# Optimization experiments

Measured on AMD Instinct MI355X. Metric: run time of the kernel, lower is better.

Reference implementation:

```python
import jax, jax.numpy as jnp
from jax import lax
import numpy as np

D_MODEL = 1024
D_STATE = 16
D_CONV = 4
EXPAND = 2
D_INNER = EXPAND * D_MODEL
BATCH = 2
SEQLEN = 1024


def setup_inputs() -> dict:
    key = jax.random.key(0)
    ks = jax.random.split(key, 8)
    x = jax.random.normal(ks[0], (BATCH, SEQLEN, D_MODEL), jnp.float32)
    W_in = jax.random.normal(ks[1], (2 * D_INNER, D_MODEL), jnp.float32) * (1.0 / np.sqrt(D_MODEL))
    conv_w = jax.random.normal(ks[2], (D_INNER, 1, D_CONV), jnp.float32) * (1.0 / np.sqrt(D_CONV))
    conv_b = jax.random.normal(ks[3], (D_INNER,), jnp.float32) * 0.02
    W_x = jax.random.normal(ks[4], (2 * D_STATE, D_INNER), jnp.float32) * (1.0 / np.sqrt(D_INNER))
    W_dt = jax.random.normal(ks[5], (D_INNER, D_INNER), jnp.float32) * (1.0 / np.sqrt(D_INNER))
    b_dt = jax.random.normal(ks[6], (D_INNER,), jnp.float32) * 0.02
    # A_log = log(arange(1..d_state)) repeated over d_inner rows, as in __init__
    A_log = jnp.log(jnp.tile(jnp.arange(1, D_STATE + 1, dtype=jnp.float32), (D_INNER, 1)))
    D = jnp.ones((D_INNER,), jnp.float32)
    W_out = jax.random.normal(ks[7], (D_MODEL, D_INNER), jnp.float32) * (1.0 / np.sqrt(D_INNER))
    return {"x": x, "W_in": W_in, "conv_w": conv_w, "conv_b": conv_b,
            "W_x": W_x, "W_dt": W_dt, "b_dt": b_dt, "A_log": A_log,
            "D": D, "W_out": W_out}


def reference(x, W_in, conv_w, conv_b, W_x, W_dt, b_dt, A_log, D, W_out):
    d_inner, _, d_conv = conv_w.shape
    d_state = A_log.shape[1]

    # in_proj and split into x / gate z
    xz = x @ W_in.T                                   # (B, L, 2*d_inner)
    xi, z = jnp.split(xz, 2, axis=-1)

    # causal depthwise conv1d: torch pads both sides by d_conv-1 then slices
    # [:seqlen], which equals left-only padding of d_conv-1
    xc = lax.conv_general_dilated(
        xi.transpose(0, 2, 1), conv_w, window_strides=(1,),
        padding=[(d_conv - 1, 0)],
        dimension_numbers=("NCH", "OIH", "NCH"),
        feature_group_count=d_inner)
    xc = xc + conv_b[None, :, None]
    u = jax.nn.silu(xc.transpose(0, 2, 1))            # (B, L, d_inner)

    # input-dependent B, C and dt
    BC = u @ W_x.T                                    # (B, L, 2*d_state)
    Bmat, Cmat = jnp.split(BC, 2, axis=-1)
    dt = jax.nn.softplus(u @ W_dt.T + b_dt)           # (B, L, d_inner)

    A = -jnp.exp(A_log)                               # (d_inner, d_state)
    dA = jnp.exp(dt[..., None] * A)                   # (B, L, d_inner, d_state)
    dBu = dt[..., None] * Bmat[:, :, None, :] * u[..., None]

    def step(s, inp):
        dA_t, dBu_t, C_t = inp
        s = dA_t * s + dBu_t                          # (B, d_inner, d_state)
        y_t = jnp.einsum("bdn,bn->bd", s, C_t)
        return s, y_t

    s0 = jnp.zeros((x.shape[0], d_inner, d_state), x.dtype)
    _, ys = lax.scan(step, s0,
                     (dA.transpose(1, 0, 2, 3),
                      dBu.transpose(1, 0, 2, 3),
                      Cmat.transpose(1, 0, 2)))
    y = ys.transpose(1, 0, 2) + D * u                 # (B, L, d_inner)

    y = y * jax.nn.silu(z)
    # dropout is identity in eval mode
    return y @ W_out.T
```

## Files before the change

### kernel.cpp

```cpp
#include <hip/hip_runtime.h>
#include <hip/hip_bf16.h>
#include <math.h>

#define B_SZ   2
#define LSEQ   1024
#define DMODEL 1024
#define DSTATE 16
#define DCONV  4
#define DINNER 2048
#define MROWS  (B_SZ * LSEQ)
#define NCHUNK 32
#define TCHUNK (LSEQ / NCHUNK)
#define NCAT   2176
#define BKS    64

typedef __attribute__((ext_vector_type(8))) short bf16x8;
typedef __attribute__((ext_vector_type(4))) float f32x4;

__device__ __forceinline__ void gl2lds16(const void* g, void* l) {
    __builtin_amdgcn_global_load_lds(
        (const __attribute__((address_space(1))) void*)g,
        (__attribute__((address_space(3))) void*)l, 16, 0, 0);
}

__device__ __forceinline__ void cvt8(const float* __restrict__ in,
                                     __hip_bfloat16* __restrict__ out, int i)
{
    float4 a = *(const float4*)&in[i];
    float4 b = *(const float4*)&in[i + 4];
    union { __hip_bfloat16 h[8]; int4 v; } o;
    o.h[0] = __float2bfloat16(a.x); o.h[1] = __float2bfloat16(a.y);
    o.h[2] = __float2bfloat16(a.z); o.h[3] = __float2bfloat16(a.w);
    o.h[4] = __float2bfloat16(b.x); o.h[5] = __float2bfloat16(b.y);
    o.h[6] = __float2bfloat16(b.z); o.h[7] = __float2bfloat16(b.w);
    *(int4*)&out[i] = o.v;
}

__global__ __launch_bounds__(256)
void cvt_all(const float* __restrict__ x,    __hip_bfloat16* __restrict__ xb,
             const float* __restrict__ win,  __hip_bfloat16* __restrict__ winb,
             const float* __restrict__ wdt,  const float* __restrict__ wx,
             __hip_bfloat16* __restrict__ wcat,
             const float* __restrict__ wout, __hip_bfloat16* __restrict__ woutb)
{
    const int b = blockIdx.x;
    const int t8 = threadIdx.x * 8;
    if      (b < 1024) cvt8(x,    xb,    b * 2048 + t8);
    else if (b < 3072) cvt8(win,  winb,  (b - 1024) * 2048 + t8);
    else if (b < 5120) cvt8(wdt,  wcat,  (b - 3072) * 2048 + t8);
    else if (b < 5152) cvt8(wx,   wcat + (size_t)DINNER * DINNER,
                                         (b - 5120) * 2048 + t8);
    else               cvt8(wout, woutb, (b - 5152) * 2048 + t8);
}

template<int EPI>
__global__ __launch_bounds__(256)
void gemm_bt(const __hip_bfloat16* __restrict__ A,
             const __hip_bfloat16* __restrict__ B,
             const float* __restrict__ bias,
             float* __restrict__ Cbase, size_t pstride, int ldc,
             __hip_bfloat16* __restrict__ Cb, float* __restrict__ C2,
             int K, int klen)
{
    constexpr int BN   = 64;
    constexpr int NLD  = (128 + BN) / 8 / 4;
    constexpr int SMEL = (128 + BN) * BKS;
    __shared__ __hip_bfloat16 sm[3 * SMEL];

    const int tid  = threadIdx.x;
    const int lane = tid & 63;
    const int w    = tid >> 6;
    const int m0 = blockIdx.x * 128;
    const int n0 = blockIdx.y * BN;
    const int wr = w >> 1, wc = w & 1;
    const int kbase = blockIdx.z * klen;
    float* __restrict__ C = Cbase + (size_t)blockIdx.z * pstride;

    const int lrow = lane >> 3;
    const int swc  = ((lane & 7) ^ lrow) * 8;
    const __hip_bfloat16* srcp[NLD];
    #pragma unroll
    for (int i = 0; i < NLD; ++i) {
        const int q = w + 4 * i;
        srcp[i] = (q < 16)
            ? A + (size_t)(m0 + q * 8 + lrow) * K + kbase + swc
            : B + (size_t)(n0 + (q - 16) * 8 + lrow) * K + kbase + swc;
    }

    f32x4 acc[4][2] = {};
    const int l7 = lane & 7, l15 = lane & 15, lq = lane >> 4;
    const int sw0 = (lq ^ l7) * 8;
    const int sw1 = sw0 ^ 32;

    const int nt = klen / BKS;
    #pragma unroll
    for (int i = 0; i < NLD; ++i)
        gl2lds16(srcp[i], sm + (w + 4 * i) * 512);
    if (nt > 1)
        #pragma unroll
        for (int i = 0; i < NLD; ++i)
            gl2lds16(srcp[i] + BKS, sm + SMEL + (w + 4 * i) * 512);

    int cb = 0;
    for (int t = 0; t < nt; ++t) {
        if (t + 1 < nt) asm volatile("s_waitcnt vmcnt(6)" ::: "memory");
        else            asm volatile("s_waitcnt vmcnt(0)" ::: "memory");
        __builtin_amdgcn_s_barrier();
        __builtin_amdgcn_sched_barrier(0);
        if (t + 2 < nt) {
            int db = cb + 2; if (db >= 3) db -= 3;
            #pragma unroll
            for (int i = 0; i < NLD; ++i)
                gl2lds16(srcp[i] + (size_t)(t + 2) * BKS,
                         sm + db * SMEL + (w + 4 * i) * 512);
        }
        const __hip_bfloat16* As = sm + cb * SMEL;
        const __hip_bfloat16* Bs = As + 128 * BKS;
        bf16x8 a0[4], a1[4], b0[2], b1[2];
        #pragma unroll
        for (int m = 0; m < 4; ++m) {
            const int r = (wr * 64 + m * 16 + l15) * BKS;
            a0[m] = *(const bf16x8*)&As[r + sw0];
            a1[m] = *(const bf16x8*)&As[r + sw1];
        }
        #pragma unroll
        for (int n = 0; n < 2; ++n) {
            const int r = (wc * 32 + n * 16 + l15) * BKS;
            b0[n] = *(const bf16x8*)&Bs[r + sw0];
            b1[n] = *(const bf16x8*)&Bs[r + sw1];
        }
        #pragma unroll
        for (int m = 0; m < 4; ++m)
            #pragma unroll
            for (int n = 0; n < 2; ++n) {
                acc[m][n] = __builtin_amdgcn_mfma_f32_16x16x32_bf16(
                    a0[m], b0[n], acc[m][n], 0, 0, 0);
                acc[m][n] = __builtin_amdgcn_mfma_f32_16x16x32_bf16(
                    a1[m], b1[n], acc[m][n], 0, 0, 0);
            }
        cb = (cb == 2) ? 0 : cb + 1;
    }

    #pragma unroll
    for (int m = 0; m < 4; ++m)
        #pragma unroll
        for (int n = 0; n < 2; ++n) {
            const int col = n0 + wc * 32 + n * 16 + l15;
            #pragma unroll
            for (int j = 0; j < 4; ++j) {
                const int row = m0 + wr * 64 + m * 16 + lq * 4 + j;
                float v = acc[m][n][j];
                if (EPI == 0) {
                    C[(size_t)row * ldc + col] = v;
                } else {
                    if (col < DINNER) {
                        v += bias[col];
                        v = (v > 20.f) ? v : log1pf(__expf(v));
                        Cb[(size_t)row * ldc + col] = __float2bfloat16(v);
                    } else if (col < DINNER + 32) {
                        C2[(size_t)row * 32 + (col - DINNER)] = v;
                    }
                }
            }
        }
}

__global__ __launch_bounds__(256)
void add2(const float* __restrict__ a, const float* __restrict__ b,
          float* __restrict__ o)
{
    int i = (blockIdx.x * 256 + threadIdx.x) * 4;
    float4 va = *(const float4*)&a[i];
    float4 vb = *(const float4*)&b[i];
    va.x += vb.x; va.y += vb.y; va.z += vb.z; va.w += vb.w;
    *(float4*)&o[i] = va;
}

__global__ __launch_bounds__(256)
void conv_silu(const float* __restrict__ xz, const float* __restrict__ cw,
               const float* __restrict__ cb, __hip_bfloat16* __restrict__ u_bf)
{
    int idx = blockIdx.x * blockDim.x + threadIdx.x;
    int d = idx & (DINNER - 1);
    int m = idx >> 11;
    int t = m & (LSEQ - 1);
    float acc = cb[d];
    #pragma unroll
    for (int j = 0; j < DCONV; ++j) {
        int tt = t - (DCONV - 1) + j;
        if (tt >= 0)
            acc += xz[(size_t)(m - t + tt) * 4096 + d] * cw[d * DCONV + j];
    }
    float v = acc / (1.f + __expf(-acc));
    u_bf[(size_t)m * DINNER + d] = __float2bfloat16(v);
}

__global__ __launch_bounds__(256)
void scan_part1(const __hip_bfloat16* __restrict__ dt,
                const __hip_bfloat16* __restrict__ u,
                const float* __restrict__ bc, const float* __restrict__ A_log,
                float* __restrict__ s_end, float* __restrict__ dtsum)
{
    const int d = blockIdx.x * 256 + threadIdx.x;
    const int c = blockIdx.y;
    const int b = blockIdx.z;
    __shared__ float bcs[TCHUNK][32];
    {
        int f = threadIdx.x * 4;
        const float* src = bc + ((size_t)b * LSEQ + c * TCHUNK) * 32;
        *(float4*)&bcs[f >> 5][f & 31] = *(const float4*)&src[f];
    }
    float An[16];
    {
        float4 a0 = *(const float4*)&A_log[d * DSTATE + 0];
        float4 a1 = *(const float4*)&A_log[d * DSTATE + 4];
        float4 a2 = *(const float4*)&A_log[d * DSTATE + 8];
        float4 a3 = *(const float4*)&A_log[d * DSTATE + 12];
        An[0]=-__expf(a0.x); An[1]=-__expf(a0.y); An[2]=-__expf(a0.z); An[3]=-__expf(a0.w);
        An[4]=-__expf(a1.x); An[5]=-__expf(a1.y); An[6]=-__expf(a1.z); An[7]=-__expf(a1.w);
        An[8]=-__expf(a2.x); An[9]=-__expf(a2.y); An[10]=-__expf(a2.z); An[11]=-__expf(a2.w);
        An[12]=-__expf(a3.x); An[13]=-__expf(a3.y); An[14]=-__expf(a3.z); An[15]=-__expf(a3.w);
    }
    __syncthreads();
    const __hip_bfloat16* dtp = dt + ((size_t)b * LSEQ + c * TCHUNK) * DINNER + d;
    const __hip_bfloat16* up  = u  + ((size_t)b * LSEQ + c * TCHUNK) * DINNER + d;
    float s[16] = {};
    float sum = 0.f;
    for (int t = 0; t < TCHUNK; ++t) {
        float dtv = __bfloat162float(dtp[(size_t)t * DINNER]);
        float uv  = __bfloat162float(up [(size_t)t * DINNER]);
        sum += dtv;
        float du = dtv * uv;
        #pragma unroll
        for (int n = 0; n < 16; ++n) {
            float a = __expf(dtv * An[n]);
            s[n] = a * s[n] + du * bcs[t][n];
        }
    }
    float* se = s_end + ((size_t)(b * NCHUNK + c) * DINNER + d) * 16;
    #pragma unroll
    for (int q = 0; q < 4; ++q)
        *(float4*)&se[q * 4] = make_float4(s[q*4], s[q*4+1], s[q*4+2], s[q*4+3]);
    dtsum[(size_t)(b * NCHUNK + c) * DINNER + d] = sum;
}

__global__ __launch_bounds__(256)
void scan_combine(float* __restrict__ s_end, const float* __restrict__ dtsum,
                  const float* __restrict__ A_log)
{
    int idx = blockIdx.x * 256 + threadIdx.x;
    int n = idx & 15;
    int d = (idx >> 4) & (DINNER - 1);
    int b = idx >> 15;
    float An = -__expf(A_log[d * DSTATE + n]);
    float s = 0.f;
    for (int c = 0; c < NCHUNK; ++c) {
        size_t base = (size_t)(b * NCHUNK + c) * DINNER + d;
        float se = s_end[base * 16 + n];
        s_end[base * 16 + n] = s;
        float P = __expf(An * dtsum[base]);
        s = P * s + se;
    }
}

__global__ __launch_bounds__(256)
void scan_part2(const __hip_bfloat16* __restrict__ dt,
                const __hip_bfloat16* __restrict__ u,
                const float* __restrict__ bc, const float* __restrict__ s_in,
                const float* __restrict__ A_log, const float* __restrict__ Dp,
                const float* __restrict__ xz, __hip_bfloat16* __restrict__ y_bf)
{
    const int d = blockIdx.x * 256 + threadIdx.x;
    const int c = blockIdx.y;
    const int b = blockIdx.z;
    __shared__ float bcs[TCHUNK][32];
    {
        int f = threadIdx.x * 4;
        const float* src = bc + ((size_t)b * LSEQ + c * TCHUNK) * 32;
        *(float4*)&bcs[f >> 5][f & 31] = *(const float4*)&src[f];
    }
    float An[16];
    {
        float4 a0 = *(const float4*)&A_log[d * DSTATE + 0];
        float4 a1 = *(const float4*)&A_log[d * DSTATE + 4];
        float4 a2 = *(const float4*)&A_log[d * DSTATE + 8];
        float4 a3 = *(const float4*)&A_log[d * DSTATE + 12];
        An[0]=-__expf(a0.x); An[1]=-__expf(a0.y); An[2]=-__expf(a0.z); An[3]=-__expf(a0.w);
        An[4]=-__expf(a1.x); An[5]=-__expf(a1.y); An[6]=-__expf(a1.z); An[7]=-__expf(a1.w);
        An[8]=-__expf(a2.x); An[9]=-__expf(a2.y); An[10]=-__expf(a2.z); An[11]=-__expf(a2.w);
        An[12]=-__expf(a3.x); An[13]=-__expf(a3.y); An[14]=-__expf(a3.z); An[15]=-__expf(a3.w);
    }
    float s[16];
    {
        const float* si = s_in + ((size_t)(b * NCHUNK + c) * DINNER + d) * 16;
        #pragma unroll
        for (int q = 0; q < 4; ++q) {
            float4 v = *(const float4*)&si[q * 4];
            s[q*4] = v.x; s[q*4+1] = v.y; s[q*4+2] = v.z; s[q*4+3] = v.w;
        }
    }
    const float Dd = Dp[d];
    __syncthreads();
    const __hip_bfloat16* dtp = dt + ((size_t)b * LSEQ + c * TCHUNK) * DINNER + d;
    const __hip_bfloat16* up  = u  + ((size_t)b * LSEQ + c * TCHUNK) * DINNER + d;
    const float* zp  = xz + ((size_t)b * LSEQ + c * TCHUNK) * 4096 + 2048 + d;
    __hip_bfloat16* yp = y_bf + ((size_t)b * LSEQ + c * TCHUNK) * DINNER + d;
    for (int t = 0; t < TCHUNK; ++t) {
        float dtv = __bfloat162float(dtp[(size_t)t * DINNER]);
        float uv  = __bfloat162float(up [(size_t)t * DINNER]);
        float du = dtv * uv;
        float y = Dd * uv;
        #pragma unroll
        for (int n = 0; n < 16; ++n) {
            float a = __expf(dtv * An[n]);
            s[n] = a * s[n] + du * bcs[t][n];
            y += s[n] * bcs[t][16 + n];
        }
        float zv = zp[(size_t)t * 4096];
        yp[(size_t)t * DINNER] = __float2bfloat16(y * (zv / (1.f + __expf(-zv))));
    }
}

extern "C" void kernel_launch(void* const* d_in, const int* in_sizes, int n_in,
                              void* d_out, int out_size, void* d_ws, size_t ws_size,
                              hipStream_t stream)
{
    const float* x      = (const float*)d_in[0];
    const float* W_in   = (const float*)d_in[1];
    const float* conv_w = (const float*)d_in[2];
    const float* conv_b = (const float*)d_in[3];
    const float* W_x    = (const float*)d_in[4];
    const float* W_dt   = (const float*)d_in[5];
    const float* b_dt   = (const float*)d_in[6];
    const float* A_log  = (const float*)d_in[7];
    const float* Dp     = (const float*)d_in[8];
    const float* W_out  = (const float*)d_in[9];
    float* out = (float*)d_out;

    const size_t MB = 1ull << 20;
    char* w8 = (char*)d_ws;
    float* xz    = (float*)(w8);
    float* p3    = (float*)(w8);
    __hip_bfloat16* u_bf  = (__hip_bfloat16*)(w8 + 32*MB);
    __hip_bfloat16* dtc   = (__hip_bfloat16*)(w8 + 40*MB);
    float* bc    = (float*)(w8 + 48*MB);
    float* sbuf  = (float*)(w8 + 49*MB);
    float* dtsum = (float*)(w8 + 57*MB);
    __hip_bfloat16* x_bf   = (__hip_bfloat16*)(w8 + 58*MB);
    __hip_bfloat16* Win_bf = (__hip_bfloat16*)(w8 + 62*MB);
    __hip_bfloat16* y_bf   = (__hip_bfloat16*)(w8 + 58*MB);
    __hip_bfloat16* Wcat_bf= (__hip_bfloat16*)(w8 + 70*MB);
    __hip_bfloat16* Wout_bf= (__hip_bfloat16*)(w8 + 78*MB + 512*1024);

    cvt_all<<<6176, 256, 0, stream>>>(x, x_bf, W_in, Win_bf,
                                      W_dt, W_x, Wcat_bf, W_out, Wout_bf);
    gemm_bt<0><<<dim3(16, 64, 1), 256, 0, stream>>>(
        x_bf, Win_bf, nullptr, xz, 0, 4096, nullptr, nullptr, DMODEL, DMODEL);
    conv_silu<<<(MROWS * DINNER) / 256, 256, 0, stream>>>(xz, conv_w, conv_b, u_bf);
    gemm_bt<2><<<dim3(16, NCAT / 64, 1), 256, 0, stream>>>(
        u_bf, Wcat_bf, b_dt, nullptr, 0, DINNER, dtc, bc, DINNER, DINNER);
    scan_part1<<<dim3(DINNER/256, NCHUNK, B_SZ), 256, 0, stream>>>(
        dtc, u_bf, bc, A_log, sbuf, dtsum);
    scan_combine<<<(B_SZ * DINNER * DSTATE) / 256, 256, 0, stream>>>(
        sbuf, dtsum, A_log);
    scan_part2<<<dim3(DINNER/256, NCHUNK, B_SZ), 256, 0, stream>>>(
        dtc, u_bf, bc, sbuf, A_log, Dp, xz, y_bf);
    gemm_bt<0><<<dim3(16, 16, 2), 256, 0, stream>>>(
        y_bf, Wout_bf, nullptr, p3, (size_t)MROWS * DMODEL, DMODEL, nullptr,
        nullptr, DINNER, DINNER / 2);
    add2<<<(MROWS * DMODEL) / 1024, 256, 0, stream>>>(
        p3, p3 + (size_t)MROWS * DMODEL, out);
}
```

Before: 184.3 us.

## Use 256x128 tiles with 512 threads for in/out projections; split-K by four

Adds a larger-tile GEMM kernel (256x128 per block, 8 waves, 4x4 MFMA tiles per wave, double-buffered LDS) for the input and output projections, and raises the output-projection split-K from two to four with a four-way reduction kernel. The dt/BC GEMM is specialised and moves from triple to double buffering with a full wait at the end of each k-step. Larger tiles raise data reuse per block but cut the block count (256 blocks for in_proj, 256 for out_proj) and occupancy. The simpler double-buffer pipeline with vmcnt(0) also exposes more load latency.

```diff
diff --git a/kernel.cpp b/kernel.cpp
--- a/kernel.cpp
+++ b/kernel.cpp
@@ -53,19 +53,110 @@
     else               cvt8(wout, woutb, (b - 5152) * 2048 + t8);
 }
 
-template<int EPI>
-__global__ __launch_bounds__(256)
-void gemm_bt(const __hip_bfloat16* __restrict__ A,
-             const __hip_bfloat16* __restrict__ B,
-             const float* __restrict__ bias,
-             float* __restrict__ Cbase, size_t pstride, int ldc,
-             __hip_bfloat16* __restrict__ Cb, float* __restrict__ C2,
-             int K, int klen)
+__global__ __launch_bounds__(512)
+void gemm_bt_big(const __hip_bfloat16* __restrict__ A,
+                 const __hip_bfloat16* __restrict__ B,
+                 float* __restrict__ Cbase, size_t pstride, int ldc,
+                 int K, int klen)
+{
+    constexpr int SMEL = (256 + 128) * BKS;
+    __shared__ __hip_bfloat16 sm[2 * SMEL];
+
+    const int tid  = threadIdx.x;
+    const int lane = tid & 63;
+    const int w    = tid >> 6;
+    const int m0 = blockIdx.x * 256;
+    const int n0 = blockIdx.y * 128;
+    const int wr = w >> 1, wc = w & 1;
+    const int kbase = blockIdx.z * klen;
+    float* __restrict__ C = Cbase + (size_t)blockIdx.z * pstride;
+
+    const int lrow = lane >> 3;
+    const int swc  = ((lane & 7) ^ lrow) * 8;
+    const __hip_bfloat16* srcp[6];
+    #pragma unroll
+    for (int i = 0; i < 6; ++i) {
+        const int q = w + 8 * i;
+        srcp[i] = (q < 32)
+            ? A + (size_t)(m0 + q * 8 + lrow) * K + kbase + swc
+            : B + (size_t)(n0 + (q - 32) * 8 + lrow) * K + kbase + swc;
+    }
+
+    f32x4 acc[4][4] = {};
+    const int l7 = lane & 7, l15 = lane & 15, lq = lane >> 4;
+    const int sw0 = (lq ^ l7) * 8;
+    const int sw1 = sw0 ^ 32;
+
+    #pragma unroll
+    for (int i = 0; i < 6; ++i)
+        gl2lds16(srcp[i], sm + (w + 8 * i) * 512);
+    asm volatile("s_waitcnt vmcnt(0)" ::: "memory");
+    __builtin_amdgcn_s_barrier();
+    __builtin_amdgcn_sched_barrier(0);
+
+    const int nt = klen / BKS;
+    int buf = 0;
+    for (int t = 0; t < nt; ++t) {
+        if (t + 1 < nt) {
+            #pragma unroll
+            for (int i = 0; i < 6; ++i)
+                gl2lds16(srcp[i] + (size_t)(t + 1) * BKS,
+                         sm + (buf ^ 1) * SMEL + (w + 8 * i) * 512);
+        }
+        const __hip_bfloat16* As = sm + buf * SMEL;
+        const __hip_bfloat16* Bs = As + 256 * BKS;
+        bf16x8 a0[4], a1[4], b0[4], b1[4];
+        #pragma unroll
+        for (int m = 0; m < 4; ++m) {
+            const int r = (wr * 64 + m * 16 + l15) * BKS;
+            a0[m] = *(const bf16x8*)&As[r + sw0];
+            a1[m] = *(const bf16x8*)&As[r + sw1];
+        }
+        #pragma unroll
+        for (int n = 0; n < 4; ++n) {
+            const int r = (wc * 64 + n * 16 + l15) * BKS;
+            b0[n] = *(const bf16x8*)&Bs[r + sw0];
+            b1[n] = *(const bf16x8*)&Bs[r + sw1];
+        }
+        #pragma unroll
+        for (int m = 0; m < 4; ++m)
+            #pragma unroll
+            for (int n = 0; n < 4; ++n) {
+                acc[m][n] = __builtin_amdgcn_mfma_f32_16x16x32_bf16(
+                    a0[m], b0[n], acc[m][n], 0, 0, 0);
+                acc[m][n] = __builtin_amdgcn_mfma_f32_16x16x32_bf16(
+                    a1[m], b1[n], acc[m][n], 0, 0, 0);
+            }
+        asm volatile("s_waitcnt vmcnt(0)" ::: "memory");
+        __builtin_amdgcn_s_barrier();
+        __builtin_amdgcn_sched_barrier(0);
+        buf ^= 1;
+    }
+
+    #pragma unroll
+    for (int m = 0; m < 4; ++m)
+        #pragma unroll
+        for (int n = 0; n < 4; ++n) {
+            const int col = n0 + wc * 64 + n * 16 + l15;
+            #pragma unroll
+            for (int j = 0; j < 4; ++j) {
+                const int row = m0 + wr * 64 + m * 16 + lq * 4 + j;
+                C[(size_t)row * ldc + col] = acc[m][n][j];
+            }
+        }
+}
+
+__global__ __launch_bounds__(256)
+void gemm_bt_dt(const __hip_bfloat16* __restrict__ A,
+                const __hip_bfloat16* __restrict__ B,
+                const float* __restrict__ bias,
+                int ldc, __hip_bfloat16* __restrict__ Cb,
+                float* __restrict__ C2, int K)
 {
     constexpr int BN   = 64;
     constexpr int NLD  = (128 + BN) / 8 / 4;
     constexpr int SMEL = (128 + BN) * BKS;
-    __shared__ __hip_bfloat16 sm[3 * SMEL];
+    __shared__ __hip_bfloat16 sm[2 * SMEL];
 
     const int tid  = threadIdx.x;
     const int lane = tid & 63;
@@ -73,8 +164,6 @@
     const int m0 = blockIdx.x * 128;
     const int n0 = blockIdx.y * BN;
     const int wr = w >> 1, wc = w & 1;
-    const int kbase = blockIdx.z * klen;
-    float* __restrict__ C = Cbase + (size_t)blockIdx.z * pstride;
 
     const int lrow = lane >> 3;
     const int swc  = ((lane & 7) ^ lrow) * 8;
@@ -83,8 +172,8 @@
     for (int i = 0; i < NLD; ++i) {
         const int q = w + 4 * i;
         srcp[i] = (q < 16)
-            ? A + (size_t)(m0 + q * 8 + lrow) * K + kbase + swc
-            : B + (size_t)(n0 + (q - 16) * 8 + lrow) * K + kbase + swc;
+            ? A + (size_t)(m0 + q * 8 + lrow) * K + swc
+            : B + (size_t)(n0 + (q - 16) * 8 + lrow) * K + swc;
     }
 
     f32x4 acc[4][2] = {};
@@ -92,29 +181,23 @@
     const int sw0 = (lq ^ l7) * 8;
     const int sw1 = sw0 ^ 32;
 
-    const int nt = klen / BKS;
     #pragma unroll
     for (int i = 0; i < NLD; ++i)
         gl2lds16(srcp[i], sm + (w + 4 * i) * 512);
-    if (nt > 1)
-        #pragma unroll
-        for (int i = 0; i < NLD; ++i)
-            gl2lds16(srcp[i] + BKS, sm + SMEL + (w + 4 * i) * 512);
-
-    int cb = 0;
+    asm volatile("s_waitcnt vmcnt(0)" ::: "memory");
+    __builtin_amdgcn_s_barrier();
+    __builtin_amdgcn_sched_barrier(0);
+
+    const int nt = K / BKS;
+    int buf = 0;
     for (int t = 0; t < nt; ++t) {
-        if (t + 1 < nt) asm volatile("s_waitcnt vmcnt(6)" ::: "memory");
-        else            asm volatile("s_waitcnt vmcnt(0)" ::: "memory");
-        __builtin_amdgcn_s_barrier();
-        __builtin_amdgcn_sched_barrier(0);
-        if (t + 2 < nt) {
-            int db = cb + 2; if (db >= 3) db -= 3;
+        if (t + 1 < nt) {
             #pragma unroll
             for (int i = 0; i < NLD; ++i)
-                gl2lds16(srcp[i] + (size_t)(t + 2) * BKS,
-                         sm + db * SMEL + (w + 4 * i) * 512);
-        }
-        const __hip_bfloat16* As = sm + cb * SMEL;
+                gl2lds16(srcp[i] + (size_t)(t + 1) * BKS,
+                         sm + (buf ^ 1) * SMEL + (w + 4 * i) * 512);
+        }
+        const __hip_bfloat16* As = sm + buf * SMEL;
         const __hip_bfloat16* Bs = As + 128 * BKS;
         bf16x8 a0[4], a1[4], b0[2], b1[2];
         #pragma unroll
@@ -138,7 +221,10 @@
                 acc[m][n] = __builtin_amdgcn_mfma_f32_16x16x32_bf16(
                     a1[m], b1[n], acc[m][n], 0, 0, 0);
             }
-        cb = (cb == 2) ? 0 : cb + 1;
+        asm volatile("s_waitcnt vmcnt(0)" ::: "memory");
+        __builtin_amdgcn_s_barrier();
+        __builtin_amdgcn_sched_barrier(0);
+        buf ^= 1;
     }
 
     #pragma unroll
@@ -150,30 +236,29 @@
             for (int j = 0; j < 4; ++j) {
                 const int row = m0 + wr * 64 + m * 16 + lq * 4 + j;
                 float v = acc[m][n][j];
-                if (EPI == 0) {
-                    C[(size_t)row * ldc + col] = v;
-                } else {
-                    if (col < DINNER) {
-                        v += bias[col];
-                        v = (v > 20.f) ? v : log1pf(__expf(v));
-                        Cb[(size_t)row * ldc + col] = __float2bfloat16(v);
-                    } else if (col < DINNER + 32) {
-                        C2[(size_t)row * 32 + (col - DINNER)] = v;
-                    }
+                if (col < DINNER) {
+                    v += bias[col];
+                    v = (v > 20.f) ? v : log1pf(__expf(v));
+                    Cb[(size_t)row * ldc + col] = __float2bfloat16(v);
+                } else if (col < DINNER + 32) {
+                    C2[(size_t)row * 32 + (col - DINNER)] = v;
                 }
             }
         }
 }
 
 __global__ __launch_bounds__(256)
-void add2(const float* __restrict__ a, const float* __restrict__ b,
-          float* __restrict__ o)
-{
+void add4(const float* __restrict__ p, float* __restrict__ o)
+{
+    const size_t S = (size_t)MROWS * DMODEL;
     int i = (blockIdx.x * 256 + threadIdx.x) * 4;
-    float4 va = *(const float4*)&a[i];
-    float4 vb = *(const float4*)&b[i];
-    va.x += vb.x; va.y += vb.y; va.z += vb.z; va.w += vb.w;
-    *(float4*)&o[i] = va;
+    float4 a = *(const float4*)&p[i];
+    float4 b = *(const float4*)&p[i + S];
+    float4 c = *(const float4*)&p[i + 2 * S];
+    float4 d = *(const float4*)&p[i + 3 * S];
+    a.x += b.x + c.x + d.x; a.y += b.y + c.y + d.y;
+    a.z += b.z + c.z + d.z; a.w += b.w + c.w + d.w;
+    *(float4*)&o[i] = a;
 }
 
 __global__ __launch_bounds__(256)
@@ -354,20 +439,19 @@
 
     cvt_all<<<6176, 256, 0, stream>>>(x, x_bf, W_in, Win_bf,
                                       W_dt, W_x, Wcat_bf, W_out, Wout_bf);
-    gemm_bt<0><<<dim3(16, 64, 1), 256, 0, stream>>>(
-        x_bf, Win_bf, nullptr, xz, 0, 4096, nullptr, nullptr, DMODEL, DMODEL);
+    gemm_bt_big<<<dim3(8, 32, 1), 512, 0, stream>>>(
+        x_bf, Win_bf, xz, 0, 4096, DMODEL, DMODEL);
     conv_silu<<<(MROWS * DINNER) / 256, 256, 0, stream>>>(xz, conv_w, conv_b, u_bf);
-    gemm_bt<2><<<dim3(16, NCAT / 64, 1), 256, 0, stream>>>(
-        u_bf, Wcat_bf, b_dt, nullptr, 0, DINNER, dtc, bc, DINNER, DINNER);
+    gemm_bt_dt<<<dim3(16, NCAT / 64, 1), 256, 0, stream>>>(
+        u_bf, Wcat_bf, b_dt, DINNER, dtc, bc, DINNER);
     scan_part1<<<dim3(DINNER/256, NCHUNK, B_SZ), 256, 0, stream>>>(
         dtc, u_bf, bc, A_log, sbuf, dtsum);
     scan_combine<<<(B_SZ * DINNER * DSTATE) / 256, 256, 0, stream>>>(
         sbuf, dtsum, A_log);
     scan_part2<<<dim3(DINNER/256, NCHUNK, B_SZ), 256, 0, stream>>>(
         dtc, u_bf, bc, sbuf, A_log, Dp, xz, y_bf);
-    gemm_bt<0><<<dim3(16, 16, 2), 256, 0, stream>>>(
-        y_bf, Wout_bf, nullptr, p3, (size_t)MROWS * DMODEL, DMODEL, nullptr,
-        nullptr, DINNER, DINNER / 2);
-    add2<<<(MROWS * DMODEL) / 1024, 256, 0, stream>>>(
-        p3, p3 + (size_t)MROWS * DMODEL, out);
-}
+    gemm_bt_big<<<dim3(8, 8, 4), 512, 0, stream>>>(
+        y_bf, Wout_bf, p3, (size_t)MROWS * DMODEL, DMODEL,
+        DINNER, DINNER / 4);
+    add4<<<(MROWS * DMODEL) / 1024, 256, 0, stream>>>(p3, out);
+}
```

Result: faster. 178.4 us (-3.2%).

## Enlarge GEMM tiles to 256x128 with 512-thread blocks and 4-way split-K

Applied to the files above, without the earlier changes.

Replaces the 128x64 GEMM with a 256x128 tile using 8 waves per block, each wave computing a 64x64 sub-tile. The aim is more data reuse per LDS load and fewer global loads for all three projections. The output projection moves from split-K of 2 to split-K of 4 to keep enough blocks, and the reduction kernel now sums four partial buffers. The trade-offs are a larger LDS footprint (about 144KB across three buffers), fewer blocks for the 2176-wide GEMM, and extra partial-sum traffic in the final add.

```diff
diff --git a/kernel.cpp b/kernel.cpp
--- a/kernel.cpp
+++ b/kernel.cpp
@@ -54,52 +54,49 @@
 }
 
 template<int EPI>
-__global__ __launch_bounds__(256)
-void gemm_bt(const __hip_bfloat16* __restrict__ A,
-             const __hip_bfloat16* __restrict__ B,
-             const float* __restrict__ bias,
-             float* __restrict__ Cbase, size_t pstride, int ldc,
-             __hip_bfloat16* __restrict__ Cb, float* __restrict__ C2,
-             int K, int klen)
-{
-    constexpr int BN   = 64;
-    constexpr int NLD  = (128 + BN) / 8 / 4;
-    constexpr int SMEL = (128 + BN) * BKS;
+__global__ __launch_bounds__(512)
+void gemm_bt_big(const __hip_bfloat16* __restrict__ A,
+                 const __hip_bfloat16* __restrict__ B,
+                 const float* __restrict__ bias,
+                 float* __restrict__ Cbase, size_t pstride, int ldc,
+                 __hip_bfloat16* __restrict__ Cb, float* __restrict__ C2,
+                 int K, int klen)
+{
+    constexpr int SMEL = (256 + 128) * BKS;
     __shared__ __hip_bfloat16 sm[3 * SMEL];
 
     const int tid  = threadIdx.x;
     const int lane = tid & 63;
     const int w    = tid >> 6;
-    const int m0 = blockIdx.x * 128;
-    const int n0 = blockIdx.y * BN;
+    const int m0 = blockIdx.x * 256;
+    const int n0 = blockIdx.y * 128;
     const int wr = w >> 1, wc = w & 1;
     const int kbase = blockIdx.z * klen;
     float* __restrict__ C = Cbase + (size_t)blockIdx.z * pstride;
 
     const int lrow = lane >> 3;
     const int swc  = ((lane & 7) ^ lrow) * 8;
-    const __hip_bfloat16* srcp[NLD];
-    #pragma unroll
-    for (int i = 0; i < NLD; ++i) {
-        const int q = w + 4 * i;
-        srcp[i] = (q < 16)
+    const __hip_bfloat16* srcp[6];
+    #pragma unroll
+    for (int i = 0; i < 6; ++i) {
+        const int q = w + 8 * i;
+        srcp[i] = (q < 32)
             ? A + (size_t)(m0 + q * 8 + lrow) * K + kbase + swc
-            : B + (size_t)(n0 + (q - 16) * 8 + lrow) * K + kbase + swc;
-    }
-
-    f32x4 acc[4][2] = {};
+            : B + (size_t)(n0 + (q - 32) * 8 + lrow) * K + kbase + swc;
+    }
+
+    f32x4 acc[4][4] = {};
     const int l7 = lane & 7, l15 = lane & 15, lq = lane >> 4;
     const int sw0 = (lq ^ l7) * 8;
     const int sw1 = sw0 ^ 32;
 
     const int nt = klen / BKS;
     #pragma unroll
-    for (int i = 0; i < NLD; ++i)
-        gl2lds16(srcp[i], sm + (w + 4 * i) * 512);
-    if (nt > 1)
-        #pragma unroll
-        for (int i = 0; i < NLD; ++i)
-            gl2lds16(srcp[i] + BKS, sm + SMEL + (w + 4 * i) * 512);
+    for (int i = 0; i < 6; ++i)
+        gl2lds16(srcp[i], sm + (w + 8 * i) * 512);
+    #pragma unroll
+    for (int i = 0; i < 6; ++i)
+        gl2lds16(srcp[i] + BKS, sm + SMEL + (w + 8 * i) * 512);
 
     int cb = 0;
     for (int t = 0; t < nt; ++t) {
@@ -110,13 +107,14 @@
         if (t + 2 < nt) {
             int db = cb + 2; if (db >= 3) db -= 3;
             #pragma unroll
-            for (int i = 0; i < NLD; ++i)
+            for (int i = 0; i < 6; ++i)
                 gl2lds16(srcp[i] + (size_t)(t + 2) * BKS,
-                         sm + db * SMEL + (w + 4 * i) * 512);
-        }
+                         sm + db * SMEL + (w + 8 * i) * 512);
+        }
+        __builtin_amdgcn_sched_barrier(0);
         const __hip_bfloat16* As = sm + cb * SMEL;
-        const __hip_bfloat16* Bs = As + 128 * BKS;
-        bf16x8 a0[4], a1[4], b0[2], b1[2];
+        const __hip_bfloat16* Bs = As + 256 * BKS;
+        bf16x8 a0[4], a1[4], b0[4], b1[4];
         #pragma unroll
         for (int m = 0; m < 4; ++m) {
             const int r = (wr * 64 + m * 16 + l15) * BKS;
@@ -124,15 +122,15 @@
             a1[m] = *(const bf16x8*)&As[r + sw1];
         }
         #pragma unroll
-        for (int n = 0; n < 2; ++n) {
-            const int r = (wc * 32 + n * 16 + l15) * BKS;
+        for (int n = 0; n < 4; ++n) {
+            const int r = (wc * 64 + n * 16 + l15) * BKS;
             b0[n] = *(const bf16x8*)&Bs[r + sw0];
             b1[n] = *(const bf16x8*)&Bs[r + sw1];
         }
         #pragma unroll
         for (int m = 0; m < 4; ++m)
             #pragma unroll
-            for (int n = 0; n < 2; ++n) {
+            for (int n = 0; n < 4; ++n) {
                 acc[m][n] = __builtin_amdgcn_mfma_f32_16x16x32_bf16(
                     a0[m], b0[n], acc[m][n], 0, 0, 0);
                 acc[m][n] = __builtin_amdgcn_mfma_f32_16x16x32_bf16(
@@ -144,8 +142,8 @@
     #pragma unroll
     for (int m = 0; m < 4; ++m)
         #pragma unroll
-        for (int n = 0; n < 2; ++n) {
-            const int col = n0 + wc * 32 + n * 16 + l15;
+        for (int n = 0; n < 4; ++n) {
+            const int col = n0 + wc * 64 + n * 16 + l15;
             #pragma unroll
             for (int j = 0; j < 4; ++j) {
                 const int row = m0 + wr * 64 + m * 16 + lq * 4 + j;
@@ -166,14 +164,17 @@
 }
 
 __global__ __launch_bounds__(256)
-void add2(const float* __restrict__ a, const float* __restrict__ b,
-          float* __restrict__ o)
-{
+void add4(const float* __restrict__ p, float* __restrict__ o)
+{
+    const size_t S = (size_t)MROWS * DMODEL;
     int i = (blockIdx.x * 256 + threadIdx.x) * 4;
-    float4 va = *(const float4*)&a[i];
-    float4 vb = *(const float4*)&b[i];
-    va.x += vb.x; va.y += vb.y; va.z += vb.z; va.w += vb.w;
-    *(float4*)&o[i] = va;
+    float4 a = *(const float4*)&p[i];
+    float4 b = *(const float4*)&p[i + S];
+    float4 c = *(const float4*)&p[i + 2 * S];
+    float4 d = *(const float4*)&p[i + 3 * S];
+    a.x += b.x + c.x + d.x; a.y += b.y + c.y + d.y;
+    a.z += b.z + c.z + d.z; a.w += b.w + c.w + d.w;
+    *(float4*)&o[i] = a;
 }
 
 __global__ __launch_bounds__(256)
@@ -354,10 +355,10 @@
 
     cvt_all<<<6176, 256, 0, stream>>>(x, x_bf, W_in, Win_bf,
                                       W_dt, W_x, Wcat_bf, W_out, Wout_bf);
-    gemm_bt<0><<<dim3(16, 64, 1), 256, 0, stream>>>(
+    gemm_bt_big<0><<<dim3(8, 32, 1), 512, 0, stream>>>(
         x_bf, Win_bf, nullptr, xz, 0, 4096, nullptr, nullptr, DMODEL, DMODEL);
     conv_silu<<<(MROWS * DINNER) / 256, 256, 0, stream>>>(xz, conv_w, conv_b, u_bf);
-    gemm_bt<2><<<dim3(16, NCAT / 64, 1), 256, 0, stream>>>(
+    gemm_bt_big<2><<<dim3(8, NCAT / 128, 1), 512, 0, stream>>>(
         u_bf, Wcat_bf, b_dt, nullptr, 0, DINNER, dtc, bc, DINNER, DINNER);
     scan_part1<<<dim3(DINNER/256, NCHUNK, B_SZ), 256, 0, stream>>>(
         dtc, u_bf, bc, A_log, sbuf, dtsum);
@@ -365,9 +366,8 @@
         sbuf, dtsum, A_log);
     scan_part2<<<dim3(DINNER/256, NCHUNK, B_SZ), 256, 0, stream>>>(
         dtc, u_bf, bc, sbuf, A_log, Dp, xz, y_bf);
-    gemm_bt<0><<<dim3(16, 16, 2), 256, 0, stream>>>(
-        y_bf, Wout_bf, nullptr, p3, (size_t)MROWS * DMODEL, DMODEL, nullptr,
-        nullptr, DINNER, DINNER / 2);
-    add2<<<(MROWS * DMODEL) / 1024, 256, 0, stream>>>(
-        p3, p3 + (size_t)MROWS * DMODEL, out);
-}
+    gemm_bt_big<0><<<dim3(8, 8, 4), 512, 0, stream>>>(
+        y_bf, Wout_bf, nullptr, p3, (size_t)MROWS * DMODEL, DMODEL,
+        nullptr, nullptr, DINNER, DINNER / 4);
+    add4<<<(MROWS * DMODEL) / 1024, 256, 0, stream>>>(p3, out);
+}
```

Measured after the change: 199.0 us. 8.0% more time.
